# Performance work log

Hardware: AMD Instinct MI355X
Metric: run time of the kernel (lower is better)

The kernel has to match this reference:

```python
import jax, jax.numpy as jnp
import numpy as np

N = 512
H = 128
L = 4
NUM_RBF = 50
CUTOFF = 5.0
NMOL = 16
OUT = 1


def setup_inputs() -> dict:
    key = jax.random.key(0)
    ks = jax.random.split(key, 12)
    s = lambda f: 1.0 / np.sqrt(f)
    atomic_numbers = jax.random.randint(ks[0], (N,), 0, 100)
    positions = jax.random.normal(ks[1], (N, 3), dtype=jnp.float32) * 2.0
    batch = jnp.sort(jax.random.randint(ks[2], (N,), 0, NMOL))
    return {
        'atomic_numbers': atomic_numbers,
        'positions': positions,
        'batch': batch,
        'embed': jax.random.normal(ks[3], (100, H), dtype=jnp.float32) * 0.1,
        'msg_w1': jax.random.normal(ks[4], (L, H + NUM_RBF + 3, H), dtype=jnp.float32) * s(H + NUM_RBF + 3),
        'msg_b1': jnp.zeros((L, H), jnp.float32),
        'msg_w2': jax.random.normal(ks[5], (L, H, H), dtype=jnp.float32) * s(H),
        'msg_b2': jnp.zeros((L, H), jnp.float32),
        'upd_w1': jax.random.normal(ks[6], (L, 2 * H, H), dtype=jnp.float32) * s(2 * H),
        'upd_b1': jnp.zeros((L, H), jnp.float32),
        'upd_w2': jax.random.normal(ks[7], (L, H, H), dtype=jnp.float32) * s(H),
        'upd_b2': jnp.zeros((L, H), jnp.float32),
        'out_w1': jax.random.normal(ks[8], (H, H // 2), dtype=jnp.float32) * s(H),
        'out_b1': jnp.zeros((H // 2,), jnp.float32),
        'out_w2': jax.random.normal(ks[9], (H // 2, OUT), dtype=jnp.float32) * s(H // 2),
        'out_b2': jnp.zeros((OUT,), jnp.float32),
    }


def _forward(atomic_numbers, positions, batch, embed, msg_w1, msg_b1, msg_w2,
             msg_b2, upd_w1, upd_b1, upd_w2, upd_b2, out_w1, out_b1, out_w2, out_b2):
    x = embed[jnp.clip(atomic_numbers, 0, 99)]                      # [N,H]
    # all-pairs geometry: row i = source, col j = target (matches repeat_interleave/repeat)
    diff = positions[:, None, :] - positions[None, :, :]            # [N,N,3]
    dist = jnp.linalg.norm(diff, axis=-1)                           # [N,N]
    not_self = jnp.arange(N)[:, None] != jnp.arange(N)[None, :]
    valid = (dist < CUTOFF) & not_self                              # [N,N] edge mask
    dirs = diff / jnp.maximum(dist, 1e-8)[..., None]                # [N,N,3]
    # gaussian RBF: centers linspace(0, cutoff, num_rbf), width = cutoff/num_rbf
    centers = jnp.linspace(0.0, CUTOFF, NUM_RBF)
    width = CUTOFF / NUM_RBF
    rbf = jnp.exp(-(dist[..., None] - centers) ** 2 / (2.0 * width ** 2))  # [N,N,50]

    for l in range(L):
        # Linear over concat([x_j, rbf, dirs]) split by input blocks (same math)
        Wx = msg_w1[l, :H]
        Wr = msg_w1[l, H:H + NUM_RBF]
        Wd = msg_w1[l, H + NUM_RBF:]
        pre = (x @ Wx)[:, None, :] \
            + jnp.einsum('ijr,rh->ijh', rbf, Wr) \
            + jnp.einsum('ijd,dh->ijh', dirs, Wd) + msg_b1[l]       # [N,N,H]
        m = jax.nn.silu(pre) @ msg_w2[l] + msg_b2[l]                # [N,N,H]
        m = jnp.where(valid[..., None], m, 0.0)
        aggr = m.sum(axis=0)                                        # scatter-add to target j
        upd_in = jnp.concatenate([x, aggr], axis=-1)                # [N,2H]
        x = x + jax.nn.silu(upd_in @ upd_w1[l] + upd_b1[l]) @ upd_w2[l] + upd_b2[l]

    # per-molecule mean pool
    sums = jax.ops.segment_sum(x, batch, num_segments=NMOL)         # [NMOL,H]
    counts = jax.ops.segment_sum(jnp.ones((N,), x.dtype), batch, num_segments=NMOL)
    pooled = sums / jnp.maximum(counts, 1.0)[:, None]
    return jax.nn.silu(pooled @ out_w1 + out_b1) @ out_w2 + out_b2  # [NMOL,OUT]


def reference(atomic_numbers, positions, batch, embed, msg_w1, msg_b1, msg_w2,
              msg_b2, upd_w1, upd_b1, upd_w2, upd_b2, out_w1, out_b1, out_w2, out_b2):
    return _forward(atomic_numbers, positions, batch, embed, msg_w1, msg_b1, msg_w2,
                    msg_b2, upd_w1, upd_b1, upd_w2, upd_b2, out_w1, out_b1, out_w2, out_b2)
```

## Files before the change

### kernel.cpp

```cpp
#include <hip/hip_runtime.h>
#include <math.h>

#define N 512
#define H 128
#define L 4
#define NUM_RBF 50
#define NMOL 16
#define SUPER 64
#define FSTRIDE 72

typedef __attribute__((ext_vector_type(8))) short short8;
typedef __attribute__((ext_vector_type(4))) float float4v;
typedef __attribute__((ext_vector_type(4))) int int4v;

__device__ __forceinline__ float silu_f(float v) {
    return v / (1.0f + __expf(-v));
}

__device__ __forceinline__ unsigned short f2bf(float f) {
    unsigned int u = __float_as_uint(f);
    unsigned int r = (u + 0x7FFFu + ((u >> 16) & 1u)) >> 16;
    return (unsigned short)r;
}

__global__ __launch_bounds__(256) void k_embed_lin(const int* __restrict__ an,
                                                   const float* __restrict__ embed,
                                                   const float* __restrict__ pos,
                                                   const float* __restrict__ wx,
                                                   const float* __restrict__ b1,
                                                   float* __restrict__ x,
                                                   float* __restrict__ a,
                                                   int* __restrict__ nbr,
                                                   int* __restrict__ ncnt) {
    int j = blockIdx.x;
    int tid = threadIdx.x;
    int lane = tid & 63;
    int wv = tid >> 6;

    __shared__ float xs[H];
    __shared__ int wsum[4];

    float pjx = pos[j * 3 + 0], pjy = pos[j * 3 + 1], pjz = pos[j * 3 + 2];

    float xv = 0.0f;
    if (tid < H) {
        int z = an[j];
        z = min(max(z, 0), 99);
        xv = embed[z * H + tid];
        xs[tid] = xv;
    }

    int total = 0;
#pragma unroll
    for (int r = 0; r < 2; r++) {
        int i = r * 256 + tid;
        float dx = pos[i * 3 + 0] - pjx;
        float dy = pos[i * 3 + 1] - pjy;
        float dz = pos[i * 3 + 2] - pjz;
        float d2 = dx * dx + dy * dy + dz * dz;
        int valid = (d2 < 25.0f) && (i != j);
        unsigned long long m = __ballot(valid);
        int pre = __popcll(m & ((1ull << lane) - 1ull));
        if (lane == 0) wsum[wv] = __popcll(m);
        __syncthreads();
        int wbase = total;
        for (int w = 0; w < 4; w++) {
            if (w < wv) wbase += wsum[w];
        }
        int newtotal = total + wsum[0] + wsum[1] + wsum[2] + wsum[3];
        if (valid) nbr[j * 512 + wbase + pre] = i;
        __syncthreads();
        total = newtotal;
    }
    int padded = (total + 63) & ~63;
    for (int s = total + tid; s < padded; s += 256) nbr[j * 512 + s] = j;
    if (tid == 0) ncnt[j] = total;

    if (tid < H) {
        int h = tid;
        float a0 = b1[h], a1 = 0.f, a2 = 0.f, a3 = 0.f;
#pragma unroll 8
        for (int k = 0; k < H; k += 4) {
            a0 += xs[k]     * wx[(k)     * H + h];
            a1 += xs[k + 1] * wx[(k + 1) * H + h];
            a2 += xs[k + 2] * wx[(k + 2) * H + h];
            a3 += xs[k + 3] * wx[(k + 3) * H + h];
        }
        x[j * H + h] = xv;
        a[j * H + h] = (a0 + a1) + (a2 + a3);
    }
}

__global__ __launch_bounds__(512) void k_layer(const float* __restrict__ a,
                                               const float* __restrict__ pos,
                                               const int* __restrict__ nbr,
                                               const int* __restrict__ ncnt,
                                               const float* __restrict__ wfeat,
                                               const float* __restrict__ w2,
                                               const float* __restrict__ b2,
                                               const float* __restrict__ u1,
                                               const float* __restrict__ ub1,
                                               const float* __restrict__ u2,
                                               const float* __restrict__ ub2,
                                               float* __restrict__ x,
                                               const float* __restrict__ wxn,
                                               const float* __restrict__ b1n,
                                               float* __restrict__ a_next) {
    int j = blockIdx.x;
    int tid = threadIdx.x;
    int g = tid >> 8;
    int t8 = tid & 255;
    int lane = tid & 63;
    int wv4 = (tid >> 6) & 3;
    int nn = lane & 15;
    int quad = lane >> 4;
    int hbase = wv4 * 32;

    __shared__ unsigned short F[2][SUPER * FSTRIDE];
    __shared__ int nidx[2][SUPER];
    __shared__ float sjp[2][H];
    __shared__ float sj[H], xj[H], ag[H], hid[H], xn[H];
    __shared__ float part[4][H];

    int cnt = ncnt[j];
    float pjx = pos[j * 3 + 0], pjy = pos[j * 3 + 1], pjz = pos[j * 3 + 2];

    if (tid < 2 * H) sjp[tid >> 7][tid & 127] = 0.0f;

    short8 bfrag[2][2];
    for (int c = 0; c < 2; c++) {
        for (int t = 0; t < 2; t++) {
            short8 b;
            int h = hbase + 16 * t + nn;
#pragma unroll
            for (int jj = 0; jj < 8; jj++) {
                int k = c * 32 + quad * 8 + jj;
                float v = (k < NUM_RBF + 3) ? wfeat[k * H + h] : 0.0f;
                b[jj] = (short)f2bf(v);
            }
            bfrag[c][t] = b;
        }
    }

    const float DELTA = 5.0f / 49.0f;
    float pacc0 = 0.0f, pacc1 = 0.0f;

    int S = (cnt + 63) >> 6;
    int rounds = (S + 1) >> 1;
    for (int r = 0; r < rounds; r++) {
        int s = 2 * r + g;
        __syncthreads();
        if (s < S) {
            int il = t8 >> 2;
            int kb = (t8 & 3) * 16;
            int ni = nbr[j * 512 + s * 64 + il];
            if ((t8 & 3) == 0) nidx[g][il] = ni;
            float dx = pos[ni * 3 + 0] - pjx;
            float dy = pos[ni * 3 + 1] - pjy;
            float dz = pos[ni * 3 + 2] - pjz;
            float d = sqrtf(dx * dx + dy * dy + dz * dz);
            float rinv = 1.0f / fmaxf(d, 1e-8f);
            unsigned short vals[16];
#pragma unroll
            for (int qq = 0; qq < 16; qq++) {
                int k = kb + qq;
                float v;
                if (k < NUM_RBF) {
                    float tt = d - (float)k * DELTA;
                    v = __expf(-50.0f * tt * tt);
                } else if (k == NUM_RBF)     v = dx * rinv;
                else if (k == NUM_RBF + 1)   v = dy * rinv;
                else if (k == NUM_RBF + 2)   v = dz * rinv;
                else                         v = 0.0f;
                vals[qq] = f2bf(v);
            }
            unsigned int* dst = (unsigned int*)&F[g][il * FSTRIDE + kb];
#pragma unroll
            for (int qq = 0; qq < 8; qq++)
                dst[qq] = (unsigned int)vals[2 * qq] | ((unsigned int)vals[2 * qq + 1] << 16);
        }
        __syncthreads();
        if (s < S) {
#pragma unroll
            for (int it = 0; it < SUPER / 16; it++) {
                int lbase = it * 16 + quad * 4;
                int4v ni4 = *(const int4v*)&nidx[g][lbase];
                float av0[4], av1[4];
#pragma unroll
                for (int rr = 0; rr < 4; rr++) {
                    av0[rr] = a[ni4[rr] * H + hbase + nn];
                    av1[rr] = a[ni4[rr] * H + hbase + 16 + nn];
                }
                short8 afrag0 = *(const short8*)&F[g][(it * 16 + nn) * FSTRIDE + 0 * 32 + quad * 8];
                short8 afrag1 = *(const short8*)&F[g][(it * 16 + nn) * FSTRIDE + 1 * 32 + quad * 8];
                float4v acc0 = {0.0f, 0.0f, 0.0f, 0.0f};
                float4v acc1 = {0.0f, 0.0f, 0.0f, 0.0f};
                acc0 = __builtin_amdgcn_mfma_f32_16x16x32_bf16(afrag0, bfrag[0][0], acc0, 0, 0, 0);
                acc0 = __builtin_amdgcn_mfma_f32_16x16x32_bf16(afrag1, bfrag[1][0], acc0, 0, 0, 0);
                acc1 = __builtin_amdgcn_mfma_f32_16x16x32_bf16(afrag0, bfrag[0][1], acc1, 0, 0, 0);
                acc1 = __builtin_amdgcn_mfma_f32_16x16x32_bf16(afrag1, bfrag[1][1], acc1, 0, 0, 0);
#pragma unroll
                for (int rr = 0; rr < 4; rr++) {
                    float vm = (s * 64 + lbase + rr < cnt) ? 1.0f : 0.0f;
                    pacc0 += vm * silu_f(acc0[rr] + av0[rr]);
                    pacc1 += vm * silu_f(acc1[rr] + av1[rr]);
                }
            }
        }
    }

    pacc0 += __shfl_xor(pacc0, 16, 64);
    pacc0 += __shfl_xor(pacc0, 32, 64);
    pacc1 += __shfl_xor(pacc1, 16, 64);
    pacc1 += __shfl_xor(pacc1, 32, 64);
    if (lane < 16) {
        sjp[g][hbase + nn]      = pacc0;
        sjp[g][hbase + 16 + nn] = pacc1;
    }
    if (tid < H) xj[tid] = x[j * H + tid];
    __syncthreads();
    if (tid < H) sj[tid] = sjp[0][tid] + sjp[1][tid];
    __syncthreads();

    int h = tid & 127;
    int grp = tid >> 7;

    {
        float p0 = 0.f, p1 = 0.f, p2 = 0.f, p3 = 0.f;
        int k0 = grp * 32;
#pragma unroll 8
        for (int k = 0; k < 32; k += 4) {
            p0 += sj[k0 + k]     * w2[(k0 + k)     * H + h];
            p1 += sj[k0 + k + 1] * w2[(k0 + k + 1) * H + h];
            p2 += sj[k0 + k + 2] * w2[(k0 + k + 2) * H + h];
            p3 += sj[k0 + k + 3] * w2[(k0 + k + 3) * H + h];
        }
        part[grp][h] = (p0 + p1) + (p2 + p3);
    }
    __syncthreads();
    if (grp == 0) ag[h] = part[0][h] + part[1][h] + part[2][h] + part[3][h] + (float)cnt * b2[h];
    __syncthreads();

    {
        const float* src = (grp < 2) ? xj : ag;
        int sbase = (grp & 1) * 64;
        int k0 = grp * 64;
        float p0 = 0.f, p1 = 0.f, p2 = 0.f, p3 = 0.f;
#pragma unroll 8
        for (int k = 0; k < 64; k += 4) {
            p0 += src[sbase + k]     * u1[(k0 + k)     * H + h];
            p1 += src[sbase + k + 1] * u1[(k0 + k + 1) * H + h];
            p2 += src[sbase + k + 2] * u1[(k0 + k + 2) * H + h];
            p3 += src[sbase + k + 3] * u1[(k0 + k + 3) * H + h];
        }
        part[grp][h] = (p0 + p1) + (p2 + p3);
    }
    __syncthreads();
    if (grp == 0) hid[h] = silu_f(part[0][h] + part[1][h] + part[2][h] + part[3][h] + ub1[h]);
    __syncthreads();

    {
        float p0 = 0.f, p1 = 0.f, p2 = 0.f, p3 = 0.f;
        int k0 = grp * 32;
#pragma unroll 8
        for (int k = 0; k < 32; k += 4) {
            p0 += hid[k0 + k]     * u2[(k0 + k)     * H + h];
            p1 += hid[k0 + k + 1] * u2[(k0 + k + 1) * H + h];
            p2 += hid[k0 + k + 2] * u2[(k0 + k + 2) * H + h];
            p3 += hid[k0 + k + 3] * u2[(k0 + k + 3) * H + h];
        }
        part[grp][h] = (p0 + p1) + (p2 + p3);
    }
    __syncthreads();
    if (grp == 0) {
        float xv = xj[h] + part[0][h] + part[1][h] + part[2][h] + part[3][h] + ub2[h];
        x[j * H + h] = xv;
        xn[h] = xv;
    }

    if (a_next != nullptr) {
        __syncthreads();
        float p0 = 0.f, p1 = 0.f, p2 = 0.f, p3 = 0.f;
        int k0 = grp * 32;
#pragma unroll 8
        for (int k = 0; k < 32; k += 4) {
            p0 += xn[k0 + k]     * wxn[(k0 + k)     * H + h];
            p1 += xn[k0 + k + 1] * wxn[(k0 + k + 1) * H + h];
            p2 += xn[k0 + k + 2] * wxn[(k0 + k + 2) * H + h];
            p3 += xn[k0 + k + 3] * wxn[(k0 + k + 3) * H + h];
        }
        part[grp][h] = (p0 + p1) + (p2 + p3);
        __syncthreads();
        if (grp == 0)
            a_next[j * H + h] = part[0][h] + part[1][h] + part[2][h] + part[3][h] + b1n[h];
    }
}

__global__ __launch_bounds__(H) void k_pool(const float* __restrict__ x,
                                            const int* __restrict__ batch,
                                            const float* __restrict__ ow1,
                                            const float* __restrict__ ob1,
                                            const float* __restrict__ ow2,
                                            const float* __restrict__ ob2,
                                            float* __restrict__ out) {
    int m = blockIdx.x;
    int h = threadIdx.x;
    __shared__ int lo_s, hi_s;
    __shared__ float pooled[H];
    __shared__ float hid[H / 2];

    if (h == 0) {
        int a = 0, b = N;
        while (a < b) { int mid = (a + b) >> 1; if (batch[mid] < m) a = mid + 1; else b = mid; }
        lo_s = a;
        b = N;
        while (a < b) { int mid = (a + b) >> 1; if (batch[mid] < m + 1) a = mid + 1; else b = mid; }
        hi_s = a;
    }
    __syncthreads();

    int lo = lo_s, hi = hi_s;
    float s = 0.0f;
    for (int i = lo; i < hi; i++) s += x[i * H + h];
    pooled[h] = s / (float)max(hi - lo, 1);
    __syncthreads();

    if (h < H / 2) {
        float p0 = 0.f, p1 = 0.f;
        for (int k = 0; k < H; k += 2) {
            p0 += pooled[k]     * ow1[(k)     * (H / 2) + h];
            p1 += pooled[k + 1] * ow1[(k + 1) * (H / 2) + h];
        }
        hid[h] = silu_f(p0 + p1 + ob1[h]);
    }
    __syncthreads();

    if (h == 0) {
        float o = ob2[0];
        for (int k = 0; k < H / 2; k++) o += hid[k] * ow2[k];
        out[m] = o;
    }
}

extern "C" void kernel_launch(void* const* d_in, const int* in_sizes, int n_in,
                              void* d_out, int out_size, void* d_ws, size_t ws_size,
                              hipStream_t stream) {
    const int*   an      = (const int*)d_in[0];
    const float* pos     = (const float*)d_in[1];
    const int*   batch   = (const int*)d_in[2];
    const float* embed   = (const float*)d_in[3];
    const float* msg_w1  = (const float*)d_in[4];
    const float* msg_b1  = (const float*)d_in[5];
    const float* msg_w2  = (const float*)d_in[6];
    const float* msg_b2  = (const float*)d_in[7];
    const float* upd_w1  = (const float*)d_in[8];
    const float* upd_b1  = (const float*)d_in[9];
    const float* upd_w2  = (const float*)d_in[10];
    const float* upd_b2  = (const float*)d_in[11];
    const float* out_w1  = (const float*)d_in[12];
    const float* out_b1  = (const float*)d_in[13];
    const float* out_w2  = (const float*)d_in[14];
    const float* out_b2  = (const float*)d_in[15];
    float* out = (float*)d_out;

    float* x    = (float*)d_ws;
    float* a0   = x + N * H;
    float* a1   = a0 + N * H;
    int*   nbr  = (int*)(a1 + N * H);
    int*   ncnt = nbr + N * 512;

    const int W1ROWS = H + NUM_RBF + 3;

    k_embed_lin<<<N, 256, 0, stream>>>(an, embed, pos, msg_w1, msg_b1, x, a0, nbr, ncnt);
    for (int l = 0; l < L; l++) {
        float* a_cur  = (l & 1) ? a1 : a0;
        float* a_next = (l + 1 < L) ? ((l & 1) ? a0 : a1) : nullptr;
        const float* wxn = (l + 1 < L) ? (msg_w1 + (l + 1) * W1ROWS * H) : nullptr;
        const float* b1n = (l + 1 < L) ? (msg_b1 + (l + 1) * H) : nullptr;
        k_layer<<<N, 512, 0, stream>>>(a_cur, pos, nbr, ncnt,
                                       msg_w1 + l * W1ROWS * H + H * H,
                                       msg_w2 + l * H * H, msg_b2 + l * H,
                                       upd_w1 + l * 2 * H * H, upd_b1 + l * H,
                                       upd_w2 + l * H * H, upd_b2 + l * H,
                                       x, wxn, b1n, a_next);
    }
    k_pool<<<NMOL, H, 0, stream>>>(x, batch, out_w1, out_b1, out_w2, out_b2, out);
}
```

Measured before the change: 230.1 us.

## Compute RBF features per wave in registers, removing shared staging and barriers

Replaces the shared-memory feature tile built cooperatively by 256 threads with per-wave register construction of MFMA A-fragments for 16-neighbor tiles. Neighbor indices are broadcast via shuffles instead of LDS. This removes the two block-wide barriers per round and the LDS writes and reads. In exchange, each of the four waves in a group recomputes the same exp-based RBF features, increasing transcendental work.

```diff
diff --git a/kernel.cpp b/kernel.cpp
--- a/kernel.cpp
+++ b/kernel.cpp
@@ -6,12 +6,9 @@
 #define L 4
 #define NUM_RBF 50
 #define NMOL 16
-#define SUPER 64
-#define FSTRIDE 72
 
 typedef __attribute__((ext_vector_type(8))) short short8;
 typedef __attribute__((ext_vector_type(4))) float float4v;
-typedef __attribute__((ext_vector_type(4))) int int4v;
 
 __device__ __forceinline__ float silu_f(float v) {
     return v / (1.0f + __expf(-v));
@@ -108,16 +105,14 @@
                                                float* __restrict__ a_next) {
     int j = blockIdx.x;
     int tid = threadIdx.x;
-    int g = tid >> 8;
-    int t8 = tid & 255;
+    int wave = tid >> 6;
+    int g2 = wave >> 2;
+    int wv4 = wave & 3;
     int lane = tid & 63;
-    int wv4 = (tid >> 6) & 3;
     int nn = lane & 15;
     int quad = lane >> 4;
     int hbase = wv4 * 32;
 
-    __shared__ unsigned short F[2][SUPER * FSTRIDE];
-    __shared__ int nidx[2][SUPER];
     __shared__ float sjp[2][H];
     __shared__ float sj[H], xj[H], ag[H], hid[H], xn[H];
     __shared__ float part[4][H];
@@ -125,7 +120,7 @@
     int cnt = ncnt[j];
     float pjx = pos[j * 3 + 0], pjy = pos[j * 3 + 1], pjz = pos[j * 3 + 2];
 
-    if (tid < 2 * H) sjp[tid >> 7][tid & 127] = 0.0f;
+    if (tid < H) xj[tid] = x[j * H + tid];
 
     short8 bfrag[2][2];
     for (int c = 0; c < 2; c++) {
@@ -145,67 +140,55 @@
     const float DELTA = 5.0f / 49.0f;
     float pacc0 = 0.0f, pacc1 = 0.0f;
 
-    int S = (cnt + 63) >> 6;
-    int rounds = (S + 1) >> 1;
-    for (int r = 0; r < rounds; r++) {
-        int s = 2 * r + g;
-        __syncthreads();
-        if (s < S) {
-            int il = t8 >> 2;
-            int kb = (t8 & 3) * 16;
-            int ni = nbr[j * 512 + s * 64 + il];
-            if ((t8 & 3) == 0) nidx[g][il] = ni;
-            float dx = pos[ni * 3 + 0] - pjx;
-            float dy = pos[ni * 3 + 1] - pjy;
-            float dz = pos[ni * 3 + 2] - pjz;
-            float d = sqrtf(dx * dx + dy * dy + dz * dz);
-            float rinv = 1.0f / fmaxf(d, 1e-8f);
-            unsigned short vals[16];
-#pragma unroll
-            for (int qq = 0; qq < 16; qq++) {
-                int k = kb + qq;
-                float v;
-                if (k < NUM_RBF) {
-                    float tt = d - (float)k * DELTA;
-                    v = __expf(-50.0f * tt * tt);
-                } else if (k == NUM_RBF)     v = dx * rinv;
-                else if (k == NUM_RBF + 1)   v = dy * rinv;
-                else if (k == NUM_RBF + 2)   v = dz * rinv;
-                else                         v = 0.0f;
-                vals[qq] = f2bf(v);
-            }
-            unsigned int* dst = (unsigned int*)&F[g][il * FSTRIDE + kb];
-#pragma unroll
-            for (int qq = 0; qq < 8; qq++)
-                dst[qq] = (unsigned int)vals[2 * qq] | ((unsigned int)vals[2 * qq + 1] << 16);
-        }
-        __syncthreads();
-        if (s < S) {
-#pragma unroll
-            for (int it = 0; it < SUPER / 16; it++) {
-                int lbase = it * 16 + quad * 4;
-                int4v ni4 = *(const int4v*)&nidx[g][lbase];
-                float av0[4], av1[4];
-#pragma unroll
-                for (int rr = 0; rr < 4; rr++) {
-                    av0[rr] = a[ni4[rr] * H + hbase + nn];
-                    av1[rr] = a[ni4[rr] * H + hbase + 16 + nn];
-                }
-                short8 afrag0 = *(const short8*)&F[g][(it * 16 + nn) * FSTRIDE + 0 * 32 + quad * 8];
-                short8 afrag1 = *(const short8*)&F[g][(it * 16 + nn) * FSTRIDE + 1 * 32 + quad * 8];
-                float4v acc0 = {0.0f, 0.0f, 0.0f, 0.0f};
-                float4v acc1 = {0.0f, 0.0f, 0.0f, 0.0f};
-                acc0 = __builtin_amdgcn_mfma_f32_16x16x32_bf16(afrag0, bfrag[0][0], acc0, 0, 0, 0);
-                acc0 = __builtin_amdgcn_mfma_f32_16x16x32_bf16(afrag1, bfrag[1][0], acc0, 0, 0, 0);
-                acc1 = __builtin_amdgcn_mfma_f32_16x16x32_bf16(afrag0, bfrag[0][1], acc1, 0, 0, 0);
-                acc1 = __builtin_amdgcn_mfma_f32_16x16x32_bf16(afrag1, bfrag[1][1], acc1, 0, 0, 0);
-#pragma unroll
-                for (int rr = 0; rr < 4; rr++) {
-                    float vm = (s * 64 + lbase + rr < cnt) ? 1.0f : 0.0f;
-                    pacc0 += vm * silu_f(acc0[rr] + av0[rr]);
-                    pacc1 += vm * silu_f(acc1[rr] + av1[rr]);
-                }
-            }
+    int T = (cnt + 15) >> 4;
+    for (int t = g2; t < T; t += 2) {
+        int ni = nbr[j * 512 + t * 16 + nn];
+        float dx = pos[ni * 3 + 0] - pjx;
+        float dy = pos[ni * 3 + 1] - pjy;
+        float dz = pos[ni * 3 + 2] - pjz;
+        float d = sqrtf(dx * dx + dy * dy + dz * dz);
+        float rinv = 1.0f / fmaxf(d, 1e-8f);
+
+        int nir[4];
+#pragma unroll
+        for (int r = 0; r < 4; r++) nir[r] = __shfl(ni, quad * 4 + r, 64);
+        float av0[4], av1[4];
+#pragma unroll
+        for (int r = 0; r < 4; r++) {
+            av0[r] = a[nir[r] * H + hbase + nn];
+            av1[r] = a[nir[r] * H + hbase + 16 + nn];
+        }
+
+        short8 af0, af1;
+#pragma unroll
+        for (int jj = 0; jj < 8; jj++) {
+            int k0 = quad * 8 + jj;
+            float t0 = d - (float)k0 * DELTA;
+            af0[jj] = (short)f2bf(__expf(-50.0f * t0 * t0));
+            int k1 = 32 + quad * 8 + jj;
+            float v1;
+            if (k1 < NUM_RBF) {
+                float t1 = d - (float)k1 * DELTA;
+                v1 = __expf(-50.0f * t1 * t1);
+            } else if (k1 == NUM_RBF)     v1 = dx * rinv;
+            else if (k1 == NUM_RBF + 1)   v1 = dy * rinv;
+            else if (k1 == NUM_RBF + 2)   v1 = dz * rinv;
+            else                          v1 = 0.0f;
+            af1[jj] = (short)f2bf(v1);
+        }
+
+        float4v acc0 = {0.0f, 0.0f, 0.0f, 0.0f};
+        float4v acc1 = {0.0f, 0.0f, 0.0f, 0.0f};
+        acc0 = __builtin_amdgcn_mfma_f32_16x16x32_bf16(af0, bfrag[0][0], acc0, 0, 0, 0);
+        acc0 = __builtin_amdgcn_mfma_f32_16x16x32_bf16(af1, bfrag[1][0], acc0, 0, 0, 0);
+        acc1 = __builtin_amdgcn_mfma_f32_16x16x32_bf16(af0, bfrag[0][1], acc1, 0, 0, 0);
+        acc1 = __builtin_amdgcn_mfma_f32_16x16x32_bf16(af1, bfrag[1][1], acc1, 0, 0, 0);
+
+#pragma unroll
+        for (int r = 0; r < 4; r++) {
+            float vm = (t * 16 + quad * 4 + r < cnt) ? 1.0f : 0.0f;
+            pacc0 += vm * silu_f(acc0[r] + av0[r]);
+            pacc1 += vm * silu_f(acc1[r] + av1[r]);
         }
     }
 
@@ -214,10 +197,9 @@
     pacc1 += __shfl_xor(pacc1, 16, 64);
     pacc1 += __shfl_xor(pacc1, 32, 64);
     if (lane < 16) {
-        sjp[g][hbase + nn]      = pacc0;
-        sjp[g][hbase + 16 + nn] = pacc1;
-    }
-    if (tid < H) xj[tid] = x[j * H + tid];
+        sjp[g2][hbase + lane]      = pacc0;
+        sjp[g2][hbase + 16 + lane] = pacc1;
+    }
     __syncthreads();
     if (tid < H) sj[tid] = sjp[0][tid] + sjp[1][tid];
     __syncthreads();
```

Result: slower. 269.1 us (+16.9%).

## Fold source-node projection into edge MFMA and rebuild neighbor list per layer

Applied to the files above, without the earlier changes.

The per-node x@Wx projection is no longer precomputed. Each edge's features now include the source node's hidden state, so the first message layer runs as one MFMA over K=192 (x, RBF, directions). The neighbor list is rebuilt in shared memory inside every layer kernel, which removes the separate embed/neighbor kernel and the global nbr/ncnt buffers. This drops the extra launch and the a-buffer gathers. In exchange it does roughly three times the MFMA work per edge, reads full x rows per neighbor, and rounds x to bf16, which may lose accuracy.

```diff
diff --git a/kernel.cpp b/kernel.cpp
--- a/kernel.cpp
+++ b/kernel.cpp
@@ -7,11 +7,12 @@
 #define NUM_RBF 50
 #define NMOL 16
 #define SUPER 64
-#define FSTRIDE 72
+#define FK 192
+#define FSTRIDE 200
+#define NKC 6
 
 typedef __attribute__((ext_vector_type(8))) short short8;
 typedef __attribute__((ext_vector_type(4))) float float4v;
-typedef __attribute__((ext_vector_type(4))) int int4v;
 
 __device__ __forceinline__ float silu_f(float v) {
     return v / (1.0f + __expf(-v));
@@ -23,37 +24,44 @@
     return (unsigned short)r;
 }
 
-__global__ __launch_bounds__(256) void k_embed_lin(const int* __restrict__ an,
-                                                   const float* __restrict__ embed,
-                                                   const float* __restrict__ pos,
-                                                   const float* __restrict__ wx,
-                                                   const float* __restrict__ b1,
-                                                   float* __restrict__ x,
-                                                   float* __restrict__ a,
-                                                   int* __restrict__ nbr,
-                                                   int* __restrict__ ncnt) {
+__global__ __launch_bounds__(512) void k_layer(const int* __restrict__ an,
+                                               const float* __restrict__ embed,
+                                               const float* __restrict__ pos,
+                                               const float* __restrict__ w1,
+                                               const float* __restrict__ b1,
+                                               const float* __restrict__ w2,
+                                               const float* __restrict__ b2,
+                                               const float* __restrict__ u1,
+                                               const float* __restrict__ ub1,
+                                               const float* __restrict__ u2,
+                                               const float* __restrict__ ub2,
+                                               const float* __restrict__ xin,
+                                               float* __restrict__ xout,
+                                               int first) {
     int j = blockIdx.x;
     int tid = threadIdx.x;
     int lane = tid & 63;
-    int wv = tid >> 6;
-
-    __shared__ float xs[H];
-    __shared__ int wsum[4];
+    int wave = tid >> 6;
+    int g = tid >> 8;
+    int t8 = tid & 255;
+    int wv4 = (tid >> 6) & 3;
+    int nn = lane & 15;
+    int quad = lane >> 4;
+    int hbase = wv4 * 32;
+
+    __shared__ unsigned short F[2][SUPER * FSTRIDE];
+    __shared__ int lnbr[N];
+    __shared__ int wsum8[8];
+    __shared__ float sjp[2][H];
+    __shared__ float sj[H], xj[H], ag[H], hid[H];
+    __shared__ float part[4][H];
 
     float pjx = pos[j * 3 + 0], pjy = pos[j * 3 + 1], pjz = pos[j * 3 + 2];
-
-    float xv = 0.0f;
-    if (tid < H) {
-        int z = an[j];
-        z = min(max(z, 0), 99);
-        xv = embed[z * H + tid];
-        xs[tid] = xv;
-    }
-
-    int total = 0;
-#pragma unroll
-    for (int r = 0; r < 2; r++) {
-        int i = r * 256 + tid;
+    const float DELTA = 5.0f / 49.0f;
+
+    int cnt;
+    {
+        int i = tid;
         float dx = pos[i * 3 + 0] - pjx;
         float dy = pos[i * 3 + 1] - pjy;
         float dz = pos[i * 3 + 2] - pjz;
@@ -61,152 +69,116 @@
         int valid = (d2 < 25.0f) && (i != j);
         unsigned long long m = __ballot(valid);
         int pre = __popcll(m & ((1ull << lane) - 1ull));
-        if (lane == 0) wsum[wv] = __popcll(m);
+        if (lane == 0) wsum8[wave] = __popcll(m);
         __syncthreads();
-        int wbase = total;
-        for (int w = 0; w < 4; w++) {
-            if (w < wv) wbase += wsum[w];
-        }
-        int newtotal = total + wsum[0] + wsum[1] + wsum[2] + wsum[3];
-        if (valid) nbr[j * 512 + wbase + pre] = i;
-        __syncthreads();
-        total = newtotal;
-    }
-    int padded = (total + 63) & ~63;
-    for (int s = total + tid; s < padded; s += 256) nbr[j * 512 + s] = j;
-    if (tid == 0) ncnt[j] = total;
+        int wbase = 0, total = 0;
+        for (int w = 0; w < 8; w++) {
+            if (w < wave) wbase += wsum8[w];
+            total += wsum8[w];
+        }
+        if (valid) lnbr[wbase + pre] = i;
+        cnt = total;
+        int padded = (cnt + 63) & ~63;
+        for (int s = cnt + tid; s < padded; s += 512) lnbr[s] = j;
+    }
 
     if (tid < H) {
-        int h = tid;
-        float a0 = b1[h], a1 = 0.f, a2 = 0.f, a3 = 0.f;
-#pragma unroll 8
-        for (int k = 0; k < H; k += 4) {
-            a0 += xs[k]     * wx[(k)     * H + h];
-            a1 += xs[k + 1] * wx[(k + 1) * H + h];
-            a2 += xs[k + 2] * wx[(k + 2) * H + h];
-            a3 += xs[k + 3] * wx[(k + 3) * H + h];
-        }
-        x[j * H + h] = xv;
-        a[j * H + h] = (a0 + a1) + (a2 + a3);
-    }
-}
-
-__global__ __launch_bounds__(512) void k_layer(const float* __restrict__ a,
-                                               const float* __restrict__ pos,
-                                               const int* __restrict__ nbr,
-                                               const int* __restrict__ ncnt,
-                                               const float* __restrict__ wfeat,
-                                               const float* __restrict__ w2,
-                                               const float* __restrict__ b2,
-                                               const float* __restrict__ u1,
-                                               const float* __restrict__ ub1,
-                                               const float* __restrict__ u2,
-                                               const float* __restrict__ ub2,
-                                               float* __restrict__ x,
-                                               const float* __restrict__ wxn,
-                                               const float* __restrict__ b1n,
-                                               float* __restrict__ a_next) {
-    int j = blockIdx.x;
-    int tid = threadIdx.x;
-    int g = tid >> 8;
-    int t8 = tid & 255;
-    int lane = tid & 63;
-    int wv4 = (tid >> 6) & 3;
-    int nn = lane & 15;
-    int quad = lane >> 4;
-    int hbase = wv4 * 32;
-
-    __shared__ unsigned short F[2][SUPER * FSTRIDE];
-    __shared__ int nidx[2][SUPER];
-    __shared__ float sjp[2][H];
-    __shared__ float sj[H], xj[H], ag[H], hid[H], xn[H];
-    __shared__ float part[4][H];
-
-    int cnt = ncnt[j];
-    float pjx = pos[j * 3 + 0], pjy = pos[j * 3 + 1], pjz = pos[j * 3 + 2];
-
-    if (tid < 2 * H) sjp[tid >> 7][tid & 127] = 0.0f;
-
-    short8 bfrag[2][2];
-    for (int c = 0; c < 2; c++) {
+        if (first) {
+            int z = an[j];
+            z = min(max(z, 0), 99);
+            xj[tid] = embed[z * H + tid];
+        } else {
+            xj[tid] = xin[j * H + tid];
+        }
+    }
+
+    short8 bfrag[NKC][2];
+    for (int c = 0; c < NKC; c++) {
         for (int t = 0; t < 2; t++) {
             short8 b;
             int h = hbase + 16 * t + nn;
 #pragma unroll
             for (int jj = 0; jj < 8; jj++) {
                 int k = c * 32 + quad * 8 + jj;
-                float v = (k < NUM_RBF + 3) ? wfeat[k * H + h] : 0.0f;
+                float v = (k < H + NUM_RBF + 3) ? w1[k * H + h] : 0.0f;
                 b[jj] = (short)f2bf(v);
             }
             bfrag[c][t] = b;
         }
     }
-
-    const float DELTA = 5.0f / 49.0f;
+    float b1h0 = b1[hbase + nn];
+    float b1h1 = b1[hbase + 16 + nn];
+
+    __syncthreads();
+
     float pacc0 = 0.0f, pacc1 = 0.0f;
 
     int S = (cnt + 63) >> 6;
     int rounds = (S + 1) >> 1;
+    int il = t8 >> 2;
+    int kb2 = (t8 & 3) * 48;
+
     for (int r = 0; r < rounds; r++) {
         int s = 2 * r + g;
-        __syncthreads();
         if (s < S) {
-            int il = t8 >> 2;
-            int kb = (t8 & 3) * 16;
-            int ni = nbr[j * 512 + s * 64 + il];
-            if ((t8 & 3) == 0) nidx[g][il] = ni;
+            int ni = lnbr[s * 64 + il];
             float dx = pos[ni * 3 + 0] - pjx;
             float dy = pos[ni * 3 + 1] - pjy;
             float dz = pos[ni * 3 + 2] - pjz;
             float d = sqrtf(dx * dx + dy * dy + dz * dz);
             float rinv = 1.0f / fmaxf(d, 1e-8f);
-            unsigned short vals[16];
-#pragma unroll
-            for (int qq = 0; qq < 16; qq++) {
-                int k = kb + qq;
-                float v;
-                if (k < NUM_RBF) {
-                    float tt = d - (float)k * DELTA;
-                    v = __expf(-50.0f * tt * tt);
-                } else if (k == NUM_RBF)     v = dx * rinv;
-                else if (k == NUM_RBF + 1)   v = dy * rinv;
-                else if (k == NUM_RBF + 2)   v = dz * rinv;
-                else                         v = 0.0f;
-                vals[qq] = f2bf(v);
+            const float* xrow;
+            if (first) {
+                int z = an[ni];
+                z = min(max(z, 0), 99);
+                xrow = embed + z * H;
+            } else {
+                xrow = xin + ni * H;
             }
-            unsigned int* dst = (unsigned int*)&F[g][il * FSTRIDE + kb];
-#pragma unroll
-            for (int qq = 0; qq < 8; qq++)
-                dst[qq] = (unsigned int)vals[2 * qq] | ((unsigned int)vals[2 * qq + 1] << 16);
+            unsigned int* dst = (unsigned int*)&F[g][il * FSTRIDE + kb2];
+#pragma unroll
+            for (int q2 = 0; q2 < 24; q2++) {
+                float v0, v1;
+                int k = kb2 + 2 * q2;
+#pragma unroll
+                for (int e = 0; e < 2; e++) {
+                    int kk = k + e;
+                    float v;
+                    if (kk < H) v = xrow[kk];
+                    else if (kk < H + NUM_RBF) {
+                        float tt = d - (float)(kk - H) * DELTA;
+                        v = __expf(-50.0f * tt * tt);
+                    } else if (kk == H + NUM_RBF)     v = dx * rinv;
+                    else if (kk == H + NUM_RBF + 1)   v = dy * rinv;
+                    else if (kk == H + NUM_RBF + 2)   v = dz * rinv;
+                    else                              v = 0.0f;
+                    if (e == 0) v0 = v; else v1 = v;
+                }
+                dst[q2] = (unsigned int)f2bf(v0) | ((unsigned int)f2bf(v1) << 16);
+            }
         }
         __syncthreads();
         if (s < S) {
 #pragma unroll
             for (int it = 0; it < SUPER / 16; it++) {
                 int lbase = it * 16 + quad * 4;
-                int4v ni4 = *(const int4v*)&nidx[g][lbase];
-                float av0[4], av1[4];
-#pragma unroll
-                for (int rr = 0; rr < 4; rr++) {
-                    av0[rr] = a[ni4[rr] * H + hbase + nn];
-                    av1[rr] = a[ni4[rr] * H + hbase + 16 + nn];
-                }
-                short8 afrag0 = *(const short8*)&F[g][(it * 16 + nn) * FSTRIDE + 0 * 32 + quad * 8];
-                short8 afrag1 = *(const short8*)&F[g][(it * 16 + nn) * FSTRIDE + 1 * 32 + quad * 8];
                 float4v acc0 = {0.0f, 0.0f, 0.0f, 0.0f};
                 float4v acc1 = {0.0f, 0.0f, 0.0f, 0.0f};
-                acc0 = __builtin_amdgcn_mfma_f32_16x16x32_bf16(afrag0, bfrag[0][0], acc0, 0, 0, 0);
-                acc0 = __builtin_amdgcn_mfma_f32_16x16x32_bf16(afrag1, bfrag[1][0], acc0, 0, 0, 0);
-                acc1 = __builtin_amdgcn_mfma_f32_16x16x32_bf16(afrag0, bfrag[0][1], acc1, 0, 0, 0);
-                acc1 = __builtin_amdgcn_mfma_f32_16x16x32_bf16(afrag1, bfrag[1][1], acc1, 0, 0, 0);
+#pragma unroll
+                for (int c = 0; c < NKC; c++) {
+                    short8 af = *(const short8*)&F[g][(it * 16 + nn) * FSTRIDE + c * 32 + quad * 8];
+                    acc0 = __builtin_amdgcn_mfma_f32_16x16x32_bf16(af, bfrag[c][0], acc0, 0, 0, 0);
+                    acc1 = __builtin_amdgcn_mfma_f32_16x16x32_bf16(af, bfrag[c][1], acc1, 0, 0, 0);
+                }
 #pragma unroll
                 for (int rr = 0; rr < 4; rr++) {
                     float vm = (s * 64 + lbase + rr < cnt) ? 1.0f : 0.0f;
-                    pacc0 += vm * silu_f(acc0[rr] + av0[rr]);
-                    pacc1 += vm * silu_f(acc1[rr] + av1[rr]);
+                    pacc0 += vm * silu_f(acc0[rr] + b1h0);
+                    pacc1 += vm * silu_f(acc1[rr] + b1h1);
                 }
             }
         }
+        __syncthreads();
     }
 
     pacc0 += __shfl_xor(pacc0, 16, 64);
@@ -214,10 +186,9 @@
     pacc1 += __shfl_xor(pacc1, 16, 64);
     pacc1 += __shfl_xor(pacc1, 32, 64);
     if (lane < 16) {
-        sjp[g][hbase + nn]      = pacc0;
-        sjp[g][hbase + 16 + nn] = pacc1;
-    }
-    if (tid < H) xj[tid] = x[j * H + tid];
+        sjp[g][hbase + lane]      = pacc0;
+        sjp[g][hbase + 16 + lane] = pacc1;
+    }
     __syncthreads();
     if (tid < H) sj[tid] = sjp[0][tid] + sjp[1][tid];
     __syncthreads();
@@ -272,28 +243,8 @@
         part[grp][h] = (p0 + p1) + (p2 + p3);
     }
     __syncthreads();
-    if (grp == 0) {
-        float xv = xj[h] + part[0][h] + part[1][h] + part[2][h] + part[3][h] + ub2[h];
-        x[j * H + h] = xv;
-        xn[h] = xv;
-    }
-
-    if (a_next != nullptr) {
-        __syncthreads();
-        float p0 = 0.f, p1 = 0.f, p2 = 0.f, p3 = 0.f;
-        int k0 = grp * 32;
-#pragma unroll 8
-        for (int k = 0; k < 32; k += 4) {
-            p0 += xn[k0 + k]     * wxn[(k0 + k)     * H + h];
-            p1 += xn[k0 + k + 1] * wxn[(k0 + k + 1) * H + h];
-            p2 += xn[k0 + k + 2] * wxn[(k0 + k + 2) * H + h];
-            p3 += xn[k0 + k + 3] * wxn[(k0 + k + 3) * H + h];
-        }
-        part[grp][h] = (p0 + p1) + (p2 + p3);
-        __syncthreads();
-        if (grp == 0)
-            a_next[j * H + h] = part[0][h] + part[1][h] + part[2][h] + part[3][h] + b1n[h];
-    }
+    if (grp == 0)
+        xout[j * H + h] = xj[h] + part[0][h] + part[1][h] + part[2][h] + part[3][h] + ub2[h];
 }
 
 __global__ __launch_bounds__(H) void k_pool(const float* __restrict__ x,
@@ -363,26 +314,21 @@
     const float* out_b2  = (const float*)d_in[15];
     float* out = (float*)d_out;
 
-    float* x    = (float*)d_ws;
-    float* a0   = x + N * H;
-    float* a1   = a0 + N * H;
-    int*   nbr  = (int*)(a1 + N * H);
-    int*   ncnt = nbr + N * 512;
+    float* xA = (float*)d_ws;
+    float* xB = xA + N * H;
 
     const int W1ROWS = H + NUM_RBF + 3;
 
-    k_embed_lin<<<N, 256, 0, stream>>>(an, embed, pos, msg_w1, msg_b1, x, a0, nbr, ncnt);
     for (int l = 0; l < L; l++) {
-        float* a_cur  = (l & 1) ? a1 : a0;
-        float* a_next = (l + 1 < L) ? ((l & 1) ? a0 : a1) : nullptr;
-        const float* wxn = (l + 1 < L) ? (msg_w1 + (l + 1) * W1ROWS * H) : nullptr;
-        const float* b1n = (l + 1 < L) ? (msg_b1 + (l + 1) * H) : nullptr;
-        k_layer<<<N, 512, 0, stream>>>(a_cur, pos, nbr, ncnt,
-                                       msg_w1 + l * W1ROWS * H + H * H,
+        const float* xin = (l == 0) ? nullptr : ((l & 1) ? xA : xB);
+        float* xout = (l & 1) ? xB : xA;
+        k_layer<<<N, 512, 0, stream>>>(an, embed, pos,
+                                       msg_w1 + l * W1ROWS * H,
+                                       msg_b1 + l * H,
                                        msg_w2 + l * H * H, msg_b2 + l * H,
                                        upd_w1 + l * 2 * H * H, upd_b1 + l * H,
                                        upd_w2 + l * H * H, upd_b2 + l * H,
-                                       x, wxn, b1n, a_next);
-    }
-    k_pool<<<NMOL, H, 0, stream>>>(x, batch, out_w1, out_b1, out_w2, out_b2, out);
-}
+                                       xin, xout, (l == 0) ? 1 : 0);
+    }
+    k_pool<<<NMOL, H, 0, stream>>>(xB, batch, out_w1, out_b1, out_w2, out_b2, out);
+}
```

Result: slower. 533.1 us (+131.7%).
